# Kernel optimization log

Measured on AMD Instinct MI355X. Metric: run time of the kernel, lower is better.

## Reference

```python
import jax, jax.numpy as jnp
import numpy as np

N = 50000   # nodes
E = 1600000 # edges
G = 256     # graphs
EPS = 1e-5  # batchnorm eps (torch default)


def _bn(h, g, b):
    # training-mode BatchNorm1d: biased batch stats
    m = h.mean(0)
    v = h.var(0)
    return (h - m) * jax.lax.rsqrt(v + EPS) * g + b


def _mlp(h, W1, b1, g, be, W2, b2):
    # Lin -> BN -> ReLU -> Lin
    h = jax.nn.relu(_bn(h @ W1 + b1, g, be))
    return h @ W2 + b2


def _scatter_mean(v, idx, n):
    s = jax.ops.segment_sum(v, idx, num_segments=n)
    c = jax.ops.segment_sum(jnp.ones((v.shape[0], 1), v.dtype), idx, num_segments=n)
    return s / jnp.maximum(c, 1.0)


def setup_inputs() -> dict:
    key = jax.random.key(0)
    ks = iter(jax.random.split(key, 32))
    d = {}
    d["x"] = jax.random.normal(next(ks), (N, 48), dtype=jnp.float32)
    d["edge_index"] = jax.random.randint(next(ks), (2, E), 0, N, dtype=jnp.int64)
    d["batch"] = jnp.sort(jax.random.randint(next(ks), (N,), 0, G, dtype=jnp.int64))

    def lin(k, fin, fout):
        kw, kb = jax.random.split(k)
        s = 1.0 / np.sqrt(fin)
        return (jax.random.uniform(kw, (fin, fout), jnp.float32, -s, s),
                jax.random.uniform(kb, (fout,), jnp.float32, -s, s))

    # input BatchNorm1d(48)
    d["bn_g"] = jnp.ones((48,), jnp.float32)
    d["bn_b"] = jnp.zeros((48,), jnp.float32)

    def mlp_params(prefix, fin, fmid, fout):
        W1, b1 = lin(next(ks), fin, fmid)
        W2, b2 = lin(next(ks), fmid, fout)
        d[prefix + "_W1"], d[prefix + "_b1"] = W1, b1
        d[prefix + "_g"] = jnp.ones((fmid,), jnp.float32)
        d[prefix + "_be"] = jnp.zeros((fmid,), jnp.float32)
        d[prefix + "_W2"], d[prefix + "_b2"] = W2, b2

    mlp_params("e", 96, 128, 128)    # EdgeBlock
    mlp_params("n1", 176, 128, 128)  # NodeBlock mlp1
    mlp_params("n2", 176, 128, 128)  # NodeBlock mlp2
    mlp_params("gl", 128, 128, 2)    # GlobalBlock
    return d


def reference(x, edge_index, batch, bn_g, bn_b,
              e_W1, e_b1, e_g, e_be, e_W2, e_b2,
              n1_W1, n1_b1, n1_g, n1_be, n1_W2, n1_b2,
              n2_W1, n2_b1, n2_g, n2_be, n2_W2, n2_b2,
              gl_W1, gl_b1, gl_g, gl_be, gl_W2, gl_b2):
    x = _bn(x, bn_g, bn_b)
    row, col = edge_index[0], edge_index[1]
    # EdgeBlock: cat(src, dest) -> MLP
    edge_attr = _mlp(jnp.concatenate([x[row], x[col]], axis=1),
                     e_W1, e_b1, e_g, e_be, e_W2, e_b2)
    # NodeBlock: cat(x[row], edge_attr) -> mlp1 -> scatter_mean(col) -> cat(x,.) -> mlp2
    m = _mlp(jnp.concatenate([x[row], edge_attr], axis=1),
             n1_W1, n1_b1, n1_g, n1_be, n1_W2, n1_b2)
    agg = _scatter_mean(m, col, N)
    x2 = _mlp(jnp.concatenate([x, agg], axis=1),
              n2_W1, n2_b1, n2_g, n2_be, n2_W2, n2_b2)
    # GlobalBlock: scatter_mean over graphs -> MLP -> [G, 2]
    u = _scatter_mean(x2, batch, G)
    u = _mlp(u, gl_W1, gl_b1, gl_g, gl_be, gl_W2, gl_b2)
    return u
```

## Files before the change

### kernel.cpp

```cpp
#include <hip/hip_runtime.h>
#include <hip/hip_bf16.h>
#include <stdint.h>

#define DEV static __device__ __forceinline__

constexpr int N_ = 50000;
constexpr int E_ = 1600000;
constexpr int G_ = 256;

typedef __attribute__((ext_vector_type(8))) short short8;
typedef __attribute__((ext_vector_type(4))) float float4v;

DEV uint16_t f2bf(float f){
  uint32_t u = __float_as_uint(f);
  uint32_t r = (u + 0x7fffu + ((u >> 16) & 1u)) >> 16;
  return (uint16_t)r;
}
DEV float bf2f(uint16_t v){ return __uint_as_float((uint32_t)v << 16); }
DEV void unpack2(uint32_t p, float& a, float& b){
  a = __uint_as_float(p << 16);
  b = __uint_as_float(p & 0xffff0000u);
}
DEV uint32_t pack2(float a, float b){
  return (uint32_t)f2bf(a) | ((uint32_t)f2bf(b) << 16);
// ... 196 lines not shown
    float4v wv = *(const float4v*)&W[k][cg*4];
    #pragma unroll
    for (int i = 0; i < 4; i++)
      #pragma unroll
      for (int j = 0; j < 4; j++)
        acc[i][j] += xv[i]*wv[j];
  }
  #pragma unroll
  for (int i = 0; i < 4; i++){
    int n = n0 + ng*4 + i;
    if (n >= N_) continue;
    uint2 pv;
    pv.x = pack2(acc[i][0], acc[i][1]);
    pv.y = pack2(acc[i][2], acc[i][3]);
    *(uint2*)&Bn[(size_t)n*128 + cg*4] = pv;
  }
}

__global__ void k_bnfin(const float* __restrict__ statsR, int reps, const float* __restrict__ g,
                        const float* __restrict__ be, float* __restrict__ s_out, float* __restrict__ t_out,
                        float inv_n){
  int c = threadIdx.x;
  if (c >= 128) return;
  float sm = 0.f, sq = 0.f;
  for (int r = 0; r < reps; r++){ sm += statsR[r*256 + c]; sq += statsR[r*256 + 128 + c]; }
  float m = sm * inv_n;
  float v = sq * inv_n - m*m;
  float s = g[c] / sqrtf(v + 1e-5f);
  s_out[c] = s;
  t_out[c] = be[c] - m*s;
}


__global__ __launch_bounds__(512, 4) void k_estats2(
    const int2* __restrict__ rcs, const uint16_t* __restrict__ xn,
    const uint16_t* __restrict__ Bn, const uint16_t* __restrict__ W1t,
    float* __restrict__ estR){
  __shared__ __align__(16) uint16_t XNR[128*68];
  __shared__ __align__(16) uint16_t Hh[128*132];
  __shared__ __align__(16) uint16_t Wb[128*68];
  __shared__ __align__(16) uint16_t Bseg[32*128];
  __shared__ float lst[256];
  __shared__ int ssid[128], scol[128], scseg[32];
  __shared__ int sm_w0, snseg;
  const int t = threadIdx.x;
  const long i0 = (long)blockIdx.x * 128;
  const int lane = t & 63, w = t >> 6;
  const int m = lane & 15, quad = lane >> 4;
  uint32_t* XNRd = (uint32_t*)XNR;
  uint32_t* Wd = (uint32_t*)Wb;
  uint32_t* Hd = (uint32_t*)Hh;

  if (t < 256) lst[t] = 0.f;

  int sid_loc = 0; bool bnd = false; int myc = 0;
  if (t < 128){
    myc = rcs[i0 + t].y;
    int prevc = (t > 0) ? rcs[i0 + t - 1].y : myc;
    bnd = (t > 0) && (myc != prevc);
    unsigned long long mask = __ballot(bnd);
    sid_loc = __popcll(mask << (63 - lane));
    scol[t] = myc;
    if (t == 63) sm_w0 = sid_loc;
  }
  {
    int e = t >> 2, q = t & 3;
    int r = rcs[i0 + e].x;
    const uint2* src = (const uint2*)(xn + (size_t)r*48 + q*12);
    uint2 d0 = src[0], d1 = src[1], d2 = src[2];
    uint32_t* dst = XNRd + e*34 + q*6;
    *(uint2*)dst = d0; *(uint2*)(dst+2) = d1; *(uint2*)(dst+4) = d2;
  }
  for (int idx = t; idx < 1024; idx += 512){
    int rr = idx >> 3;
    XNRd[rr*34 + 24 + (idx & 7)] = 0;
  }
  {
    const uint32_t* src = (const uint32_t*)W1t;
    for (int idx = t; idx < 4096; idx += 512){
      int n = idx >> 5, d = idx & 31;
      Wd[n*34 + d] = src[n*32 + d];
    }
  }
  __syncthreads();
  if (t >= 64 && t < 128) sid_loc += sm_w0;
  if (t < 128){
    ssid[t] = sid_loc;
    if ((bnd || t == 0) && sid_loc < 32) scseg[sid_loc] = myc;
    if (t == 127) snseg = sid_loc + 1;
  }
  __syncthreads();
  {
    int ns = snseg; if (ns > 32) ns = 32;
    uint32_t* Bsegd = (uint32_t*)Bseg;
    const uint32_t* Bnd = (const uint32_t*)Bn;
    for (int idx = t; idx < ns*64; idx += 512){
      int s = idx >> 6, d = idx & 63;
      Bsegd[s*64 + d] = Bnd[(size_t)scseg[s]*64 + d];
    }
  }
  __syncthreads();

  float4v acc[8];
  #pragma unroll
  for (int nt = 0; nt < 8; nt++){ acc[nt][0]=0.f; acc[nt][1]=0.f; acc[nt][2]=0.f; acc[nt][3]=0.f; }
  {
    const uint16_t* aptr = XNR + (w*16 + m)*68 + quad*8;
    const uint16_t* bbase = Wb + m*68 + quad*8;
    #pragma unroll
    for (int ks = 0; ks < 2; ks++){
      short8 af = lds_load8(aptr + ks*32);
      #pragma unroll
      for (int nt = 0; nt < 8; nt++){
        short8 bf = lds_load8(bbase + nt*16*68 + ks*32);
        acc[nt] = __builtin_amdgcn_mfma_f32_16x16x32_bf16(af, bf, acc[nt], 0, 0, 0);
      }
    }
  }
  {
    int elb = w*16 + quad*4;
    int sids[4];
    #pragma unroll
    for (int reg = 0; reg < 4; reg++) sids[reg] = ssid[elb + reg];
    #pragma unroll
    for (int nt = 0; nt < 8; nt++){
      int col = nt*16 + m;
      #pragma unroll
      for (int reg = 0; reg < 4; reg++){
        float b = (sids[reg] < 32) ? bf2f(Bseg[sids[reg]*128 + col])
                                   : bf2f(Bn[(size_t)scol[elb+reg]*128 + col]);
        Hh[(elb+reg)*132 + col] = f2bf(acc[nt][reg] + b);
      }
    }
  }
  __syncthreads();
  {
    int cp = t & 63, eg = t >> 6;
    float ss0=0,qq0=0,ss1=0,qq1=0;
    #pragma unroll
    for (int it = 0; it < 16; it++){
      int e = it*8 + eg;
      uint32_t ph = Hd[e*66 + cp];
      float h0,h1; unpack2(ph,h0,h1);
      ss0 += h0; qq0 += h0*h0; ss1 += h1; qq1 += h1*h1;
    }
    atomicAdd(&lst[2*cp], ss0);
    atomicAdd(&lst[2*cp+1], ss1);
    atomicAdd(&lst[128+2*cp], qq0);
    atomicAdd(&lst[128+2*cp+1], qq1);
  }
  __syncthreads();
  if (t < 256) atomicAdd(&estR[(blockIdx.x & 63)*256 + t], lst[t]);
}

__global__ __launch_bounds__(512, 4) void k_epass0(
    const int2* __restrict__ rcs, const uint16_t* __restrict__ xn,
    const uint16_t* __restrict__ Bn, const uint16_t* __restrict__ W1t,
    const uint16_t* __restrict__ Mt, const uint16_t* __restrict__ N1t,
    const float* __restrict__ se, const float* __restrict__ te,
    float* __restrict__ n1R){
  __shared__ __align__(16) uint16_t XNR[128*68];
  __shared__ __align__(16) uint16_t Hh[128*132];
  __shared__ __align__(16) uint16_t Wb[128*68];
  __shared__ __align__(16) uint16_t Bseg[32*128];
  __shared__ float sete[256];
  __shared__ float lst[256];
  __shared__ int ssid[128], scol[128], scseg[32];
  __shared__ int sm_w0, snseg;
  const int t = threadIdx.x;
  const long i0 = (long)blockIdx.x * 128;
  const int lane = t & 63, w = t >> 6;
  const int m = lane & 15, quad = lane >> 4;
  uint32_t* XNRd = (uint32_t*)XNR;
  uint32_t* Wd = (uint32_t*)Wb;
  uint32_t* Hd = (uint32_t*)Hh;

  if (t < 256) lst[t] = 0.f;
  if (t < 128){ sete[t] = se[t]; sete[128 + t] = te[t]; }

  int sid_loc = 0; bool bnd = false; int myc = 0;
  if (t < 128){
    myc = rcs[i0 + t].y;
    int prevc = (t > 0) ? rcs[i0 + t - 1].y : myc;
    bnd = (t > 0) && (myc != prevc);
    unsigned long long mask = __ballot(bnd);
    sid_loc = __popcll(mask << (63 - lane));
    scol[t] = myc;
    if (t == 63) sm_w0 = sid_loc;
  }
  {
    int e = t >> 2, q = t & 3;
    int r = rcs[i0 + e].x;
    const uint2* src = (const uint2*)(xn + (size_t)r*48 + q*12);
    uint2 d0 = src[0], d1 = src[1], d2 = src[2];
    uint32_t* dst = XNRd + e*34 + q*6;
    *(uint2*)dst = d0; *(uint2*)(dst+2) = d1; *(uint2*)(dst+4) = d2;
  }
  for (int idx = t; idx < 1024; idx += 512){
    int rr = idx >> 3;
    XNRd[rr*34 + 24 + (idx & 7)] = 0;
  }
  {
    const uint32_t* src = (const uint32_t*)W1t;
    for (int idx = t; idx < 4096; idx += 512){
      int n = idx >> 5, d = idx & 31;
      Wd[n*34 + d] = src[n*32 + d];
    }
  }
  __syncthreads();
  if (t >= 64 && t < 128) sid_loc += sm_w0;
  if (t < 128){
    ssid[t] = sid_loc;
    if ((bnd || t == 0) && sid_loc < 32) scseg[sid_loc] = myc;
    if (t == 127) snseg = sid_loc + 1;
  }
  __syncthreads();
  {
    int ns = snseg; if (ns > 32) ns = 32;
    uint32_t* Bsegd = (uint32_t*)Bseg;
    const uint32_t* Bnd = (const uint32_t*)Bn;
    for (int idx = t; idx < ns*64; idx += 512){
      int s = idx >> 6, d = idx & 63;
      Bsegd[s*64 + d] = Bnd[(size_t)scseg[s]*64 + d];
    }
  }
  __syncthreads();

  float4v acc[8];
  #pragma unroll
  for (int nt = 0; nt < 8; nt++){ acc[nt][0]=0.f; acc[nt][1]=0.f; acc[nt][2]=0.f; acc[nt][3]=0.f; }
  {
    const uint16_t* aptr = XNR + (w*16 + m)*68 + quad*8;
    const uint16_t* bbase = Wb + m*68 + quad*8;
    #pragma unroll
    for (int ks = 0; ks < 2; ks++){
      short8 af = lds_load8(aptr + ks*32);
      #pragma unroll
      for (int nt = 0; nt < 8; nt++){
        short8 bf = lds_load8(bbase + nt*16*68 + ks*32);
        acc[nt] = __builtin_amdgcn_mfma_f32_16x16x32_bf16(af, bf, acc[nt], 0, 0, 0);
      }
    }
  }
  {
    int elb = w*16 + quad*4;
    int sids[4];
    #pragma unroll
    for (int reg = 0; reg < 4; reg++) sids[reg] = ssid[elb + reg];
    #pragma unroll
    for (int nt = 0; nt < 8; nt++){
      int col = nt*16 + m;
      float sc = sete[col], tc = sete[128 + col];
      #pragma unroll
      for (int reg = 0; reg < 4; reg++){
        float b = (sids[reg] < 32) ? bf2f(Bseg[sids[reg]*128 + col])
                                   : bf2f(Bn[(size_t)scol[elb+reg]*128 + col]);
        float v = fmaxf(0.f, (acc[nt][reg] + b)*sc + tc);
        Hh[(elb+reg)*132 + col] = f2bf(v);
      }
    }
  }

  float4v acc2[8];
  #pragma unroll
  for (int nt = 0; nt < 8; nt++){ acc2[nt][0]=0.f; acc2[nt][1]=0.f; acc2[nt][2]=0.f; acc2[nt][3]=0.f; }
  const uint32_t* Mtd = (const uint32_t*)Mt;
  const uint32_t* N1td = (const uint32_t*)N1t;
  for (int s = 0; s < 3; s++){
    __syncthreads();
    for (int idx = t; idx < 4096; idx += 512){
      int n = idx >> 5, d = idx & 31;
      Wd[n*34 + d] = (s < 2) ? Mtd[n*64 + s*32 + d] : N1td[n*32 + d];
    }
    __syncthreads();
    const uint16_t* a2 = (s == 2) ? (XNR + (w*16 + m)*68 + quad*8)
                                  : (Hh + (w*16 + m)*132 + s*64 + quad*8);
    const uint16_t* bbase = Wb + m*68 + quad*8;
    #pragma unroll
    for (int ks = 0; ks < 2; ks++){
      short8 af = lds_load8(a2 + ks*32);
      #pragma unroll
      for (int nt = 0; nt < 8; nt++){
        short8 bf = lds_load8(bbase + nt*16*68 + ks*32);
        acc2[nt] = __builtin_amdgcn_mfma_f32_16x16x32_bf16(af, bf, acc2[nt], 0, 0, 0);
      }
    }
  }
  __syncthreads();
  {
    int elb = w*16 + quad*4;
    #pragma unroll
    for (int nt = 0; nt < 8; nt++)
      #pragma unroll
      for (int reg = 0; reg < 4; reg++)
        Hh[(elb+reg)*132 + nt*16 + m] = f2bf(acc2[nt][reg]);
  }
  __syncthreads();
  {
    int cp = t & 63, eg = t >> 6;
    float ss0=0,qq0=0,ss1=0,qq1=0;
    #pragma unroll
    for (int it = 0; it < 16; it++){
      int e = it*8 + eg;
      uint32_t ph = Hd[e*66 + cp];
      float h0,h1; unpack2(ph,h0,h1);
      ss0 += h0; qq0 += h0*h0; ss1 += h1; qq1 += h1*h1;
    }
    atomicAdd(&lst[2*cp], ss0);
    atomicAdd(&lst[2*cp+1], ss1);
    atomicAdd(&lst[128+2*cp], qq0);
    atomicAdd(&lst[128+2*cp+1], qq1);
  }
  __syncthreads();
  if (t < 256) atomicAdd(&n1R[(blockIdx.x & 63)*256 + t], lst[t]);
}

__global__ __launch_bounds__(512, 4) void k_epass1(
    const int2* __restrict__ rcs, const uint16_t* __restrict__ xn,
    const uint16_t* __restrict__ Bn, const uint16_t* __restrict__ W1t,
    const uint16_t* __restrict__ Mt, const uint16_t* __restrict__ N1t,
    const float* __restrict__ se, const float* __restrict__ te,
    const float* __restrict__ sn1, const float* __restrict__ tn1,
    float* __restrict__ aggf){
  __shared__ __align__(16) uint16_t XNR[128*68];
  __shared__ __align__(16) uint16_t Hh[128*132];
  __shared__ __align__(16) uint16_t Wb[128*68];
  __shared__ __align__(16) uint16_t Bseg[32*128];
  __shared__ float sete[256];
  __shared__ int ssid[128], scol[128], scseg[32];
  __shared__ int sm_w0, snseg;
  const int t = threadIdx.x;
  const long i0 = (long)blockIdx.x * 128;
  const int lane = t & 63, w = t >> 6;
  const int m = lane & 15, quad = lane >> 4;
  uint32_t* XNRd = (uint32_t*)XNR;
  uint32_t* Wd = (uint32_t*)Wb;
  uint32_t* Hd = (uint32_t*)Hh;
  float* segacc = (float*)Wb;

  if (t < 128){ sete[t] = se[t]; sete[128 + t] = te[t]; }

  int sid_loc = 0; bool bnd = false; int myc = 0;
  if (t < 128){
    myc = rcs[i0 + t].y;
    int prevc = (t > 0) ? rcs[i0 + t - 1].y : myc;
    bnd = (t > 0) && (myc != prevc);
    unsigned long long mask = __ballot(bnd);
    sid_loc = __popcll(mask << (63 - lane));
    scol[t] = myc;
    if (t == 63) sm_w0 = sid_loc;
  }
  {
    int e = t >> 2, q = t & 3;
    int r = rcs[i0 + e].x;
    const uint2* src = (const uint2*)(xn + (size_t)r*48 + q*12);
    uint2 d0 = src[0], d1 = src[1], d2 = src[2];
    uint32_t* dst = XNRd + e*34 + q*6;
    *(uint2*)dst = d0; *(uint2*)(dst+2) = d1; *(uint2*)(dst+4) = d2;
  }
  for (int idx = t; idx < 1024; idx += 512){
    int rr = idx >> 3;
    XNRd[rr*34 + 24 + (idx & 7)] = 0;
  }
  {
    const uint32_t* src = (const uint32_t*)W1t;
    for (int idx = t; idx < 4096; idx += 512){
      int n = idx >> 5, d = idx & 31;
      Wd[n*34 + d] = src[n*32 + d];
    }
  }
  __syncthreads();
  if (t >= 64 && t < 128) sid_loc += sm_w0;
  if (t < 128){
    ssid[t] = sid_loc;
    if ((bnd || t == 0) && sid_loc < 32) scseg[sid_loc] = myc;
    if (t == 127) snseg = sid_loc + 1;
  }
  __syncthreads();
  {
    int ns = snseg; if (ns > 32) ns = 32;
    uint32_t* Bsegd = (uint32_t*)Bseg;
    const uint32_t* Bnd = (const uint32_t*)Bn;
    for (int idx = t; idx < ns*64; idx += 512){
      int s = idx >> 6, d = idx & 63;
      Bsegd[s*64 + d] = Bnd[(size_t)scseg[s]*64 + d];
    }
  }
  __syncthreads();

  float4v acc[8];
  #pragma unroll
  for (int nt = 0; nt < 8; nt++){ acc[nt][0]=0.f; acc[nt][1]=0.f; acc[nt][2]=0.f; acc[nt][3]=0.f; }
  {
    const uint16_t* aptr = XNR + (w*16 + m)*68 + quad*8;
    const uint16_t* bbase = Wb + m*68 + quad*8;
    #pragma unroll
    for (int ks = 0; ks < 2; ks++){
      short8 af = lds_load8(aptr + ks*32);
      #pragma unroll
      for (int nt = 0; nt < 8; nt++){
        short8 bf = lds_load8(bbase + nt*16*68 + ks*32);
        acc[nt] = __builtin_amdgcn_mfma_f32_16x16x32_bf16(af, bf, acc[nt], 0, 0, 0);
      }
    }
  }
  {
    int elb = w*16 + quad*4;
    int sids[4];
    #pragma unroll
    for (int reg = 0; reg < 4; reg++) sids[reg] = ssid[elb + reg];
    #pragma unroll
    for (int nt = 0; nt < 8; nt++){
      int col = nt*16 + m;
      float sc = sete[col], tc = sete[128 + col];
      #pragma unroll
      for (int reg = 0; reg < 4; reg++){
        float b = (sids[reg] < 32) ? bf2f(Bseg[sids[reg]*128 + col])
                                   : bf2f(Bn[(size_t)scol[elb+reg]*128 + col]);
        float v = fmaxf(0.f, (acc[nt][reg] + b)*sc + tc);
        Hh[(elb+reg)*132 + col] = f2bf(v);
      }
    }
  }

  float4v acc2[8];
  #pragma unroll
  for (int nt = 0; nt < 8; nt++){ acc2[nt][0]=0.f; acc2[nt][1]=0.f; acc2[nt][2]=0.f; acc2[nt][3]=0.f; }
  const uint32_t* Mtd = (const uint32_t*)Mt;
  const uint32_t* N1td = (const uint32_t*)N1t;
  for (int s = 0; s < 3; s++){
    __syncthreads();
    for (int idx = t; idx < 4096; idx += 512){
      int n = idx >> 5, d = idx & 31;
      Wd[n*34 + d] = (s < 2) ? Mtd[n*64 + s*32 + d] : N1td[n*32 + d];
    }
    __syncthreads();
    const uint16_t* a2 = (s == 2) ? (XNR + (w*16 + m)*68 + quad*8)
                                  : (Hh + (w*16 + m)*132 + s*64 + quad*8);
    const uint16_t* bbase = Wb + m*68 + quad*8;
    #pragma unroll
    for (int ks = 0; ks < 2; ks++){
      short8 af = lds_load8(a2 + ks*32);
      #pragma unroll
      for (int nt = 0; nt < 8; nt++){
        short8 bf = lds_load8(bbase + nt*16*68 + ks*32);
        acc2[nt] = __builtin_amdgcn_mfma_f32_16x16x32_bf16(af, bf, acc2[nt], 0, 0, 0);
      }
    }
  }
  __syncthreads();
  {
    int elb = w*16 + quad*4;
    #pragma unroll
    for (int nt = 0; nt < 8; nt++)
      #pragma unroll
      for (int reg = 0; reg < 4; reg++)
        Hh[(elb+reg)*132 + nt*16 + m] = f2bf(acc2[nt][reg]);
  }
  if (t < 128){ sete[t] = sn1[t]; sete[128 + t] = tn1[t]; }
  for (int idx = t; idx < 32*128; idx += 512) segacc[idx] = 0.f;
  __syncthreads();

  {
    int cp = t & 63, eg = t >> 6;
    float s0 = sete[2*cp], s1 = sete[2*cp+1];
    float b0 = sete[128+2*cp], b1 = sete[128+2*cp+1];
    int nseg = snseg;
    bool lp = (nseg <= 32);
    int cursid = ssid[eg*16];
    int curcol = scol[eg*16];
    float r0 = 0.f, r1 = 0.f;
    for (int it = 0; it < 16; it++){
      int e = eg*16 + it;
      uint32_t ph = Hd[e*66 + cp];
      float h0,h1; unpack2(ph,h0,h1);
      float v0 = fmaxf(0.f, h0*s0 + b0);
      float v1 = fmaxf(0.f, h1*s1 + b1);
      int sid = ssid[e];
      if (sid != cursid){
        if (lp){ atomicAdd(&segacc[cursid*128 + 2*cp], r0); atomicAdd(&segacc[cursid*128 + 2*cp+1], r1); }
        else { atomicAdd(&aggf[(size_t)curcol*128 + 2*cp], r0); atomicAdd(&aggf[(size_t)curcol*128 + 2*cp+1], r1); }
        cursid = sid; curcol = scol[e]; r0 = 0.f; r1 = 0.f;
      }
      r0 += v0; r1 += v1;
    }
    if (lp){ atomicAdd(&segacc[cursid*128 + 2*cp], r0); atomicAdd(&segacc[cursid*128 + 2*cp+1], r1); }
    else { atomicAdd(&aggf[(size_t)curcol*128 + 2*cp], r0); atomicAdd(&aggf[(size_t)curcol*128 + 2*cp+1], r1); }
    __syncthreads();
    if (lp){
      for (int idx = t; idx < nseg*64; idx += 512){
        int s = idx >> 6, cpp = idx & 63;
        float v0 = segacc[s*128 + 2*cpp], v1 = segacc[s*128 + 2*cpp+1];
        int c = scseg[s];
        float* dst = &aggf[(size_t)c*128 + 2*cpp];
        if (s == 0 || s == nseg - 1){ atomicAdd(dst, v0); atomicAdd(dst+1, v1); }
        else { dst[0] = v0; dst[1] = v1; }
      }
    }
  }
}

__global__ __launch_bounds__(256) void k_n2(const float* __restrict__ x,
    const float* __restrict__ sx, const float* __restrict__ tx,
    const float* __restrict__ aggf, const float* __restrict__ invc,
    const float* __restrict__ Wc, const float* __restrict__ c1, const int* __restrict__ counts,
    float* __restrict__ hn2, float* __restrict__ n2R){
  __shared__ float xT[44][36];
  __shared__ float wT[44][128];
  __shared__ float lst[256];
  int t = threadIdx.x;
  int n0 = blockIdx.x * 32;
  int cg = t & 31, ng = t >> 5;
  lst[t] = 0.f;
  float acc[4][4] = {{0.f}};
  for (int kc = 0; kc < 176; kc += 44){
    __syncthreads();
    for (int idx = t; idx < 32*44; idx += 256){
      int r = idx / 44, k = idx % 44;
      int n = n0 + r, kk = kc + k;
      float v = 0.f;
      if (n < N_){
        if (kk < 48) v = x[(size_t)n*48 + kk] * sx[kk] + tx[kk];
        else         v = aggf[(size_t)n*128 + (kk - 48)] * invc[n];
      }
      xT[k][r] = v;
    }
    for (int idx = t; idx < 44*128; idx += 256){
      int k = idx >> 7, c = idx & 127;
      wT[k][c] = Wc[(kc + k)*128 + c];
    }
    __syncthreads();
// ... 132 lines not shown
  int* offs = (int*)take((N_+1)*4);
  int* cur  = (int*)take(N_*4);
  int* goff = (int*)take(257*4);
  int* bsum = (int*)take(64*4);
  int* boff = (int*)take(64*4);
  uint16_t* Mt  = (uint16_t*)take(128*128*2);
  uint16_t* W1t = (uint16_t*)take(128*64*2);
  uint16_t* N1t = (uint16_t*)take(128*64*2);
  uint16_t* xn  = (uint16_t*)take((size_t)N_*48*2);
  uint16_t* Bn  = (uint16_t*)take((size_t)N_*128*2);
  float* aggf  = (float*)take((size_t)N_*128*4);
  float* hn2   = (float*)take((size_t)N_*128*4);
  int2* rcs = (int2*)take((size_t)E_*8);

  if (off > ws_size) return;

  hipMemsetAsync(zone, 0, ZONE_WORDS*4, stream);
  hipMemsetAsync(aggf, 0, (size_t)N_*128*4, stream);

  const int NB = (N_ + 1023) / 1024;
  hipLaunchKernelGGL(k_xstats, dim3(252), dim3(256), 0, stream, x, xstats);
  hipLaunchKernelGGL(k_hist, dim3((E_+255)/256), dim3(256), 0, stream, ei, counts);
  hipLaunchKernelGGL(k_xfin, dim3(1), dim3(64), 0, stream, xstats, bn_g, bn_b, sx, tx);
  hipLaunchKernelGGL(k_scanA, dim3(NB), dim3(256), 0, stream, counts, bsum);
  hipLaunchKernelGGL(k_scanB, dim3(1), dim3(64), 0, stream, bsum, boff, offs, NB);
  hipLaunchKernelGGL(k_scanC, dim3(NB), dim3(256), 0, stream, counts, boff, offs, cur);
  hipLaunchKernelGGL(k_place, dim3((E_+255)/256), dim3(256), 0, stream, ei, cur, rcs);
  hipLaunchKernelGGL(k_invc, dim3((N_+255)/256), dim3(256), 0, stream, counts, invc);
  hipLaunchKernelGGL(k_wprep, dim3(281), dim3(256), 0, stream,
                     eW1, eW2, n1W1, n1W2, n2W1, n2W2, glW1, n1b2, n2b2,
                     Mt, Wcomb, M3, c1, c3, W1t, N1t);
  hipLaunchKernelGGL(k_nodegemm, dim3((N_+31)/32), dim3(256), 0, stream,
                     x, sx, tx, eW1, Bn, xn);
  hipLaunchKernelGGL(k_estats2, dim3(E_/128), dim3(512), 0, stream,
                     rcs, xn, Bn, W1t, estR);
  hipLaunchKernelGGL(k_bnfin, dim3(1), dim3(128), 0, stream, estR, 64, e_g, e_be, se, te, 1.f/(float)E_);
  hipLaunchKernelGGL(k_epass0, dim3(E_/128), dim3(512), 0, stream,
                     rcs, xn, Bn, W1t, Mt, N1t, se, te, n1R);
  hipLaunchKernelGGL(k_bnfin, dim3(1), dim3(128), 0, stream, n1R, 64, n1_g, n1_be, sn1, tn1, 1.f/(float)E_);
  hipLaunchKernelGGL(k_epass1, dim3(E_/128), dim3(512), 0, stream,
                     rcs, xn, Bn, W1t, Mt, N1t, se, te, sn1, tn1, aggf);
  hipLaunchKernelGGL(k_n2, dim3((N_+31)/32), dim3(256), 0, stream,
                     x, sx, tx, aggf, invc, Wcomb, c1, counts, hn2, n2R);
  hipLaunchKernelGGL(k_bnfin, dim3(1), dim3(128), 0, stream, n2R, 64, n2_g, n2_be, sn2, tn2, 1.f/(float)N_);
  hipLaunchKernelGGL(k_goff, dim3(1), dim3(256), 0, stream, batch, goff);
  hipLaunchKernelGGL(k_gmean, dim3(256), dim3(128), 0, stream, hn2, goff, sn2, tn2, gmean);
  hipLaunchKernelGGL(k_hg, dim3(128), dim3(256), 0, stream, gmean, M3, c3, goff, hg, gls);
  hipLaunchKernelGGL(k_bnfin, dim3(1), dim3(128), 0, stream, gls, 1, gl_g, gl_be, sgl, tgl, 1.f/(float)G_);
  hipLaunchKernelGGL(k_out, dim3(2), dim3(256), 0, stream, hg, sgl, tgl, glW2, glb2, out);
}
```

Before: 1.656 ms.

## Shrink edge-kernel tiles to 64 edges and fuse xn/N1 GEMM into first stage

The three edge-pass kernels now process 64 edges per 256-thread block instead of 128 per 512. This cuts shared memory per block, removes several block-wide barriers and lets each wave own its 16 rows through the stats and scatter phases. In epass0/epass1 the N1 projection of x[row] is computed together with the W1 GEMM from a combined weight buffer, and the M weights are loaded once as a full K=128 panel rather than in three staged chunks. Epass1 drops the shared-memory segment accumulator and atomically adds per-wave segment partials straight to global memory. That may raise global atomic traffic, and weight staging is now repeated across twice as many blocks.

```diff
diff --git a/kernel.cpp b/kernel.cpp
--- a/kernel.cpp
+++ b/kernel.cpp
@@ -252,71 +252,56 @@
 }
 
 
-__global__ __launch_bounds__(512, 4) void k_estats2(
+__global__ __launch_bounds__(256, 4) void k_estats2(
     const int2* __restrict__ rcs, const uint16_t* __restrict__ xn,
     const uint16_t* __restrict__ Bn, const uint16_t* __restrict__ W1t,
     float* __restrict__ estR){
-  __shared__ __align__(16) uint16_t XNR[128*68];
-  __shared__ __align__(16) uint16_t Hh[128*132];
-  __shared__ __align__(16) uint16_t Wb[128*68];
-  __shared__ __align__(16) uint16_t Bseg[32*128];
+  __shared__ __align__(16) uint16_t bufA[64*132];
+  __shared__ __align__(16) uint16_t bufW[128*68];
+  __shared__ __align__(16) uint16_t Bseg[8*128];
   __shared__ float lst[256];
-  __shared__ int ssid[128], scol[128], scseg[32];
-  __shared__ int sm_w0, snseg;
-  const int t = threadIdx.x;
-  const long i0 = (long)blockIdx.x * 128;
-  const int lane = t & 63, w = t >> 6;
+  __shared__ int ssid[64], scol[64], scseg[8];
+  const int t = threadIdx.x, lane = t & 63, w = t >> 6;
   const int m = lane & 15, quad = lane >> 4;
-  uint32_t* XNRd = (uint32_t*)XNR;
-  uint32_t* Wd = (uint32_t*)Wb;
-  uint32_t* Hd = (uint32_t*)Hh;
-
-  if (t < 256) lst[t] = 0.f;
-
-  int sid_loc = 0; bool bnd = false; int myc = 0;
-  if (t < 128){
-    myc = rcs[i0 + t].y;
-    int prevc = (t > 0) ? rcs[i0 + t - 1].y : myc;
-    bnd = (t > 0) && (myc != prevc);
+  const int e = t >> 2, q = t & 3;
+  const long i0 = (long)blockIdx.x * 64;
+  uint32_t* bufAd = (uint32_t*)bufA;
+
+  int r = rcs[i0 + e].x;
+  uint2 g0, g1, g2, g3;
+  if (q < 3){
+    const uint2* src = (const uint2*)(xn + (size_t)r*48 + q*16);
+    g0 = src[0]; g1 = src[1]; g2 = src[2]; g3 = src[3];
+  }
+  lst[t] = 0.f;
+  {
+    uint32_t* dst = bufAd + e*66 + q*8;
+    if (q < 3){ *(uint2*)dst = g0; *(uint2*)(dst+2) = g1; *(uint2*)(dst+4) = g2; *(uint2*)(dst+6) = g3; }
+    else { uint2 z = make_uint2(0,0); *(uint2*)dst = z; *(uint2*)(dst+2) = z; *(uint2*)(dst+4) = z; *(uint2*)(dst+6) = z; }
+  }
+  if (t < 64){
+    int myc = rcs[i0 + t].y;
+    int prevc = __shfl_up(myc, 1);
+    bool bnd = (lane > 0) && (myc != prevc);
     unsigned long long mask = __ballot(bnd);
-    sid_loc = __popcll(mask << (63 - lane));
-    scol[t] = myc;
-    if (t == 63) sm_w0 = sid_loc;
-  }
-  {
-    int e = t >> 2, q = t & 3;
-    int r = rcs[i0 + e].x;
-    const uint2* src = (const uint2*)(xn + (size_t)r*48 + q*12);
-    uint2 d0 = src[0], d1 = src[1], d2 = src[2];
-    uint32_t* dst = XNRd + e*34 + q*6;
-    *(uint2*)dst = d0; *(uint2*)(dst+2) = d1; *(uint2*)(dst+4) = d2;
-  }
-  for (int idx = t; idx < 1024; idx += 512){
-    int rr = idx >> 3;
-    XNRd[rr*34 + 24 + (idx & 7)] = 0;
-  }
-  {
-    const uint32_t* src = (const uint32_t*)W1t;
-    for (int idx = t; idx < 4096; idx += 512){
-      int n = idx >> 5, d = idx & 31;
-      Wd[n*34 + d] = src[n*32 + d];
-    }
-  }
-  __syncthreads();
-  if (t >= 64 && t < 128) sid_loc += sm_w0;
-  if (t < 128){
-    ssid[t] = sid_loc;
-    if ((bnd || t == 0) && sid_loc < 32) scseg[sid_loc] = myc;
-    if (t == 127) snseg = sid_loc + 1;
-  }
-  __syncthreads();
-  {
-    int ns = snseg; if (ns > 32) ns = 32;
+    int sid = __popcll(mask << (63 - lane));
+    int ns = __popcll(mask) + 1;
+    ssid[t] = sid; scol[t] = myc;
+    if ((bnd || lane == 0) && sid < 8) scseg[sid] = myc;
+    int nsc = (ns < 8) ? ns : 8;
+    const uint32_t* Bnd = (const uint32_t*)Bn;
     uint32_t* Bsegd = (uint32_t*)Bseg;
-    const uint32_t* Bnd = (const uint32_t*)Bn;
-    for (int idx = t; idx < ns*64; idx += 512){
+    for (int idx = lane; idx < nsc*64; idx += 64){
       int s = idx >> 6, d = idx & 63;
       Bsegd[s*64 + d] = Bnd[(size_t)scseg[s]*64 + d];
+    }
+  }
+  {
+    const uint32_t* W1d = (const uint32_t*)W1t;
+    uint32_t* Wd = (uint32_t*)bufW;
+    for (int idx = t; idx < 4096; idx += 256){
+      int n = idx >> 5, d = idx & 31;
+      Wd[n*34 + d] = W1d[n*32 + d];
     }
   }
   __syncthreads();
@@ -325,43 +310,41 @@
   #pragma unroll
   for (int nt = 0; nt < 8; nt++){ acc[nt][0]=0.f; acc[nt][1]=0.f; acc[nt][2]=0.f; acc[nt][3]=0.f; }
   {
-    const uint16_t* aptr = XNR + (w*16 + m)*68 + quad*8;
-    const uint16_t* bbase = Wb + m*68 + quad*8;
+    const uint16_t* aX = bufA + (w*16 + m)*132 + quad*8;
+    const uint16_t* bb = bufW + m*68 + quad*8;
     #pragma unroll
     for (int ks = 0; ks < 2; ks++){
-      short8 af = lds_load8(aptr + ks*32);
+      short8 af = lds_load8(aX + ks*32);
       #pragma unroll
       for (int nt = 0; nt < 8; nt++){
-        short8 bf = lds_load8(bbase + nt*16*68 + ks*32);
+        short8 bf = lds_load8(bb + nt*16*68 + ks*32);
         acc[nt] = __builtin_amdgcn_mfma_f32_16x16x32_bf16(af, bf, acc[nt], 0, 0, 0);
       }
     }
   }
   {
-    int elb = w*16 + quad*4;
-    int sids[4];
-    #pragma unroll
-    for (int reg = 0; reg < 4; reg++) sids[reg] = ssid[elb + reg];
+    const int elb = w*16 + quad*4;
+    int sid_r[4], col_r[4];
+    #pragma unroll
+    for (int reg = 0; reg < 4; reg++){ sid_r[reg] = ssid[elb + reg]; col_r[reg] = scol[elb + reg]; }
     #pragma unroll
     for (int nt = 0; nt < 8; nt++){
       int col = nt*16 + m;
       #pragma unroll
       for (int reg = 0; reg < 4; reg++){
-        float b = (sids[reg] < 32) ? bf2f(Bseg[sids[reg]*128 + col])
-                                   : bf2f(Bn[(size_t)scol[elb+reg]*128 + col]);
-        Hh[(elb+reg)*132 + col] = f2bf(acc[nt][reg] + b);
-      }
-    }
-  }
-  __syncthreads();
-  {
-    int cp = t & 63, eg = t >> 6;
+        float b = (sid_r[reg] < 8) ? bf2f(Bseg[sid_r[reg]*128 + col])
+                                   : bf2f(Bn[(size_t)col_r[reg]*128 + col]);
+        bufA[(elb + reg)*132 + col] = f2bf(acc[nt][reg] + b);
+      }
+    }
+  }
+  {
+    int cp = lane;
     float ss0=0,qq0=0,ss1=0,qq1=0;
     #pragma unroll
     for (int it = 0; it < 16; it++){
-      int e = it*8 + eg;
-      uint32_t ph = Hd[e*66 + cp];
-      float h0,h1; unpack2(ph,h0,h1);
+      uint32_t ph = bufAd[(w*16 + it)*66 + cp];
+      float h0, h1; unpack2(ph, h0, h1);
       ss0 += h0; qq0 += h0*h0; ss1 += h1; qq1 += h1*h1;
     }
     atomicAdd(&lst[2*cp], ss0);
@@ -370,160 +353,150 @@
     atomicAdd(&lst[128+2*cp+1], qq1);
   }
   __syncthreads();
-  if (t < 256) atomicAdd(&estR[(blockIdx.x & 63)*256 + t], lst[t]);
-}
-
-__global__ __launch_bounds__(512, 4) void k_epass0(
+  atomicAdd(&estR[(blockIdx.x & 63)*256 + t], lst[t]);
+}
+
+__global__ __launch_bounds__(256, 3) void k_epass0(
     const int2* __restrict__ rcs, const uint16_t* __restrict__ xn,
     const uint16_t* __restrict__ Bn, const uint16_t* __restrict__ W1t,
-    const uint16_t* __restrict__ Mt, const uint16_t* __restrict__ N1t,
+    const uint16_t* __restrict__ N1t, const uint16_t* __restrict__ Mt,
     const float* __restrict__ se, const float* __restrict__ te,
     float* __restrict__ n1R){
-  __shared__ __align__(16) uint16_t XNR[128*68];
-  __shared__ __align__(16) uint16_t Hh[128*132];
-  __shared__ __align__(16) uint16_t Wb[128*68];
-  __shared__ __align__(16) uint16_t Bseg[32*128];
-  __shared__ float sete[256];
-  __shared__ float lst[256];
-  __shared__ int ssid[128], scol[128], scseg[32];
-  __shared__ int sm_w0, snseg;
-  const int t = threadIdx.x;
-  const long i0 = (long)blockIdx.x * 128;
-  const int lane = t & 63, w = t >> 6;
+  __shared__ __align__(16) uint16_t bufA[64*132];
+  __shared__ __align__(16) uint16_t bufB[128*132];
+  __shared__ __align__(16) uint16_t Bseg[8*128];
+  __shared__ int ssid[64], scol[64], scseg[8];
+  const int t = threadIdx.x, lane = t & 63, w = t >> 6;
   const int m = lane & 15, quad = lane >> 4;
-  uint32_t* XNRd = (uint32_t*)XNR;
-  uint32_t* Wd = (uint32_t*)Wb;
-  uint32_t* Hd = (uint32_t*)Hh;
-
-  if (t < 256) lst[t] = 0.f;
-  if (t < 128){ sete[t] = se[t]; sete[128 + t] = te[t]; }
-
-  int sid_loc = 0; bool bnd = false; int myc = 0;
-  if (t < 128){
-    myc = rcs[i0 + t].y;
-    int prevc = (t > 0) ? rcs[i0 + t - 1].y : myc;
-    bnd = (t > 0) && (myc != prevc);
+  const int e = t >> 2, q = t & 3;
+  const long i0 = (long)blockIdx.x * 64;
+  uint32_t* bufAd = (uint32_t*)bufA;
+  uint32_t* bufBd = (uint32_t*)bufB;
+  float* lst = (float*)Bseg;
+
+  float se_v[8], te_v[8];
+  #pragma unroll
+  for (int nt = 0; nt < 8; nt++){ se_v[nt] = se[nt*16 + m]; te_v[nt] = te[nt*16 + m]; }
+
+  int r = rcs[i0 + e].x;
+  uint2 g0, g1, g2, g3;
+  if (q < 3){
+    const uint2* src = (const uint2*)(xn + (size_t)r*48 + q*16);
+    g0 = src[0]; g1 = src[1]; g2 = src[2]; g3 = src[3];
+  }
+  {
+    uint32_t* dst = bufAd + e*66 + q*8;
+    if (q < 3){ *(uint2*)dst = g0; *(uint2*)(dst+2) = g1; *(uint2*)(dst+4) = g2; *(uint2*)(dst+6) = g3; }
+    else { uint2 z = make_uint2(0,0); *(uint2*)dst = z; *(uint2*)(dst+2) = z; *(uint2*)(dst+4) = z; *(uint2*)(dst+6) = z; }
+  }
+  if (t < 64){
+    int myc = rcs[i0 + t].y;
+    int prevc = __shfl_up(myc, 1);
+    bool bnd = (lane > 0) && (myc != prevc);
     unsigned long long mask = __ballot(bnd);
-    sid_loc = __popcll(mask << (63 - lane));
-    scol[t] = myc;
-    if (t == 63) sm_w0 = sid_loc;
-  }
-  {
-    int e = t >> 2, q = t & 3;
-    int r = rcs[i0 + e].x;
-    const uint2* src = (const uint2*)(xn + (size_t)r*48 + q*12);
-    uint2 d0 = src[0], d1 = src[1], d2 = src[2];
-    uint32_t* dst = XNRd + e*34 + q*6;
-    *(uint2*)dst = d0; *(uint2*)(dst+2) = d1; *(uint2*)(dst+4) = d2;
-  }
-  for (int idx = t; idx < 1024; idx += 512){
-    int rr = idx >> 3;
-    XNRd[rr*34 + 24 + (idx & 7)] = 0;
-  }
-  {
-    const uint32_t* src = (const uint32_t*)W1t;
-    for (int idx = t; idx < 4096; idx += 512){
-      int n = idx >> 5, d = idx & 31;
-      Wd[n*34 + d] = src[n*32 + d];
-    }
-  }
-  __syncthreads();
-  if (t >= 64 && t < 128) sid_loc += sm_w0;
-  if (t < 128){
-    ssid[t] = sid_loc;
-    if ((bnd || t == 0) && sid_loc < 32) scseg[sid_loc] = myc;
-    if (t == 127) snseg = sid_loc + 1;
-  }
-  __syncthreads();
-  {
-    int ns = snseg; if (ns > 32) ns = 32;
+    int sid = __popcll(mask << (63 - lane));
+    int ns = __popcll(mask) + 1;
+    ssid[t] = sid; scol[t] = myc;
+    if ((bnd || lane == 0) && sid < 8) scseg[sid] = myc;
+    int nsc = (ns < 8) ? ns : 8;
+    const uint32_t* Bnd = (const uint32_t*)Bn;
     uint32_t* Bsegd = (uint32_t*)Bseg;
-    const uint32_t* Bnd = (const uint32_t*)Bn;
-    for (int idx = t; idx < ns*64; idx += 512){
+    for (int idx = lane; idx < nsc*64; idx += 64){
       int s = idx >> 6, d = idx & 63;
       Bsegd[s*64 + d] = Bnd[(size_t)scseg[s]*64 + d];
     }
   }
-  __syncthreads();
-
-  float4v acc[8];
+  {
+    const uint32_t* W1d = (const uint32_t*)W1t;
+    const uint32_t* N1d = (const uint32_t*)N1t;
+    for (int idx = t; idx < 8192; idx += 256){
+      int n = idx >> 6, d = idx & 63;
+      bufBd[n*66 + d] = (d < 32) ? W1d[n*32 + d] : N1d[n*32 + (d - 32)];
+    }
+  }
+  __syncthreads();
+
+  float4v acc1[8], acc2[8];
   #pragma unroll
-  for (int nt = 0; nt < 8; nt++){ acc[nt][0]=0.f; acc[nt][1]=0.f; acc[nt][2]=0.f; acc[nt][3]=0.f; }
-  {
-    const uint16_t* aptr = XNR + (w*16 + m)*68 + quad*8;
-    const uint16_t* bbase = Wb + m*68 + quad*8;
+  for (int nt = 0; nt < 8; nt++){
+    acc1[nt][0]=0.f; acc1[nt][1]=0.f; acc1[nt][2]=0.f; acc1[nt][3]=0.f;
+    acc2[nt][0]=0.f; acc2[nt][1]=0.f; acc2[nt][2]=0.f; acc2[nt][3]=0.f;
+  }
+  {
+    const uint16_t* aX = bufA + (w*16 + m)*132 + quad*8;
+    const uint16_t* b1 = bufB + m*132 + quad*8;
+    const uint16_t* b2 = bufB + m*132 + 64 + quad*8;
     #pragma unroll
     for (int ks = 0; ks < 2; ks++){
-      short8 af = lds_load8(aptr + ks*32);
+      short8 af = lds_load8(aX + ks*32);
       #pragma unroll
       for (int nt = 0; nt < 8; nt++){
-        short8 bf = lds_load8(bbase + nt*16*68 + ks*32);
-        acc[nt] = __builtin_amdgcn_mfma_f32_16x16x32_bf16(af, bf, acc[nt], 0, 0, 0);
-      }
-    }
-  }
-  {
-    int elb = w*16 + quad*4;
-    int sids[4];
-    #pragma unroll
-    for (int reg = 0; reg < 4; reg++) sids[reg] = ssid[elb + reg];
+        short8 bf = lds_load8(b1 + nt*16*132 + ks*32);
+        acc1[nt] = __builtin_amdgcn_mfma_f32_16x16x32_bf16(af, bf, acc1[nt], 0, 0, 0);
+      }
+      #pragma unroll
+      for (int nt = 0; nt < 8; nt++){
+        short8 bf = lds_load8(b2 + nt*16*132 + ks*32);
+        acc2[nt] = __builtin_amdgcn_mfma_f32_16x16x32_bf16(af, bf, acc2[nt], 0, 0, 0);
+      }
+    }
+  }
+  {
+    const int elb = w*16 + quad*4;
+    int sid_r[4], col_r[4];
+    #pragma unroll
+    for (int reg = 0; reg < 4; reg++){ sid_r[reg] = ssid[elb + reg]; col_r[reg] = scol[elb + reg]; }
     #pragma unroll
     for (int nt = 0; nt < 8; nt++){
       int col = nt*16 + m;
-      float sc = sete[col], tc = sete[128 + col];
       #pragma unroll
       for (int reg = 0; reg < 4; reg++){
-        float b = (sids[reg] < 32) ? bf2f(Bseg[sids[reg]*128 + col])
-                                   : bf2f(Bn[(size_t)scol[elb+reg]*128 + col]);
-        float v = fmaxf(0.f, (acc[nt][reg] + b)*sc + tc);
-        Hh[(elb+reg)*132 + col] = f2bf(v);
-      }
-    }
-  }
-
-  float4v acc2[8];
-  #pragma unroll
-  for (int nt = 0; nt < 8; nt++){ acc2[nt][0]=0.f; acc2[nt][1]=0.f; acc2[nt][2]=0.f; acc2[nt][3]=0.f; }
-  const uint32_t* Mtd = (const uint32_t*)Mt;
-  const uint32_t* N1td = (const uint32_t*)N1t;
-  for (int s = 0; s < 3; s++){
-    __syncthreads();
-    for (int idx = t; idx < 4096; idx += 512){
-      int n = idx >> 5, d = idx & 31;
-      Wd[n*34 + d] = (s < 2) ? Mtd[n*64 + s*32 + d] : N1td[n*32 + d];
-    }
-    __syncthreads();
-    const uint16_t* a2 = (s == 2) ? (XNR + (w*16 + m)*68 + quad*8)
-                                  : (Hh + (w*16 + m)*132 + s*64 + quad*8);
-    const uint16_t* bbase = Wb + m*68 + quad*8;
-    #pragma unroll
-    for (int ks = 0; ks < 2; ks++){
-      short8 af = lds_load8(a2 + ks*32);
+        float b = (sid_r[reg] < 8) ? bf2f(Bseg[sid_r[reg]*128 + col])
+                                   : bf2f(Bn[(size_t)col_r[reg]*128 + col]);
+        float v = fmaxf(0.f, (acc1[nt][reg] + b)*se_v[nt] + te_v[nt]);
+        bufA[(elb + reg)*132 + col] = f2bf(v);
+      }
+    }
+  }
+  __syncthreads();
+  {
+    const uint32_t* Mtd = (const uint32_t*)Mt;
+    for (int idx = t; idx < 8192; idx += 256){
+      int n = idx >> 6, d = idx & 63;
+      bufBd[n*66 + d] = Mtd[n*64 + d];
+    }
+  }
+  lst[t] = 0.f;
+  __syncthreads();
+
+  {
+    const uint16_t* aH = bufA + (w*16 + m)*132 + quad*8;
+    const uint16_t* bb = bufB + m*132 + quad*8;
+    #pragma unroll
+    for (int ks = 0; ks < 4; ks++){
+      short8 af = lds_load8(aH + ks*32);
       #pragma unroll
       for (int nt = 0; nt < 8; nt++){
-        short8 bf = lds_load8(bbase + nt*16*68 + ks*32);
+        short8 bf = lds_load8(bb + nt*16*132 + ks*32);
         acc2[nt] = __builtin_amdgcn_mfma_f32_16x16x32_bf16(af, bf, acc2[nt], 0, 0, 0);
       }
     }
   }
-  __syncthreads();
-  {
-    int elb = w*16 + quad*4;
+  {
+    const int elb = w*16 + quad*4;
     #pragma unroll
     for (int nt = 0; nt < 8; nt++)
       #pragma unroll
       for (int reg = 0; reg < 4; reg++)
-        Hh[(elb+reg)*132 + nt*16 + m] = f2bf(acc2[nt][reg]);
-  }
-  __syncthreads();
-  {
-    int cp = t & 63, eg = t >> 6;
+        bufA[(elb + reg)*132 + nt*16 + m] = f2bf(acc2[nt][reg]);
+  }
+  {
+    int cp = lane;
     float ss0=0,qq0=0,ss1=0,qq1=0;
     #pragma unroll
     for (int it = 0; it < 16; it++){
-      int e = it*8 + eg;
-      uint32_t ph = Hd[e*66 + cp];
-      float h0,h1; unpack2(ph,h0,h1);
+      uint32_t ph = bufAd[(w*16 + it)*66 + cp];
+      float h0, h1; unpack2(ph, h0, h1);
       ss0 += h0; qq0 += h0*h0; ss1 += h1; qq1 += h1*h1;
     }
     atomicAdd(&lst[2*cp], ss0);
@@ -532,191 +505,168 @@
     atomicAdd(&lst[128+2*cp+1], qq1);
   }
   __syncthreads();
-  if (t < 256) atomicAdd(&n1R[(blockIdx.x & 63)*256 + t], lst[t]);
-}
-
-__global__ __launch_bounds__(512, 4) void k_epass1(
+  atomicAdd(&n1R[(blockIdx.x & 63)*256 + t], lst[t]);
+}
+
+__global__ __launch_bounds__(256, 3) void k_epass1(
     const int2* __restrict__ rcs, const uint16_t* __restrict__ xn,
     const uint16_t* __restrict__ Bn, const uint16_t* __restrict__ W1t,
-    const uint16_t* __restrict__ Mt, const uint16_t* __restrict__ N1t,
+    const uint16_t* __restrict__ N1t, const uint16_t* __restrict__ Mt,
     const float* __restrict__ se, const float* __restrict__ te,
     const float* __restrict__ sn1, const float* __restrict__ tn1,
     float* __restrict__ aggf){
-  __shared__ __align__(16) uint16_t XNR[128*68];
-  __shared__ __align__(16) uint16_t Hh[128*132];
-  __shared__ __align__(16) uint16_t Wb[128*68];
-  __shared__ __align__(16) uint16_t Bseg[32*128];
-  __shared__ float sete[256];
-  __shared__ int ssid[128], scol[128], scseg[32];
-  __shared__ int sm_w0, snseg;
-  const int t = threadIdx.x;
-  const long i0 = (long)blockIdx.x * 128;
-  const int lane = t & 63, w = t >> 6;
+  __shared__ __align__(16) uint16_t bufA[64*132];
+  __shared__ __align__(16) uint16_t bufB[128*132];
+  __shared__ __align__(16) uint16_t Bseg[8*128];
+  __shared__ int ssid[64], scol[64], scseg[8];
+  const int t = threadIdx.x, lane = t & 63, w = t >> 6;
   const int m = lane & 15, quad = lane >> 4;
-  uint32_t* XNRd = (uint32_t*)XNR;
-  uint32_t* Wd = (uint32_t*)Wb;
-  uint32_t* Hd = (uint32_t*)Hh;
-  float* segacc = (float*)Wb;
-
-  if (t < 128){ sete[t] = se[t]; sete[128 + t] = te[t]; }
-
-  int sid_loc = 0; bool bnd = false; int myc = 0;
-  if (t < 128){
-    myc = rcs[i0 + t].y;
-    int prevc = (t > 0) ? rcs[i0 + t - 1].y : myc;
-    bnd = (t > 0) && (myc != prevc);
+  const int e = t >> 2, q = t & 3;
+  const long i0 = (long)blockIdx.x * 64;
+  uint32_t* bufAd = (uint32_t*)bufA;
+  uint32_t* bufBd = (uint32_t*)bufB;
+
+  float se_v[8], te_v[8], sn_v[8], tn_v[8];
+  #pragma unroll
+  for (int nt = 0; nt < 8; nt++){
+    se_v[nt] = se[nt*16 + m]; te_v[nt] = te[nt*16 + m];
+    sn_v[nt] = sn1[nt*16 + m]; tn_v[nt] = tn1[nt*16 + m];
+  }
+
+  int r = rcs[i0 + e].x;
+  uint2 g0, g1, g2, g3;
+  if (q < 3){
+    const uint2* src = (const uint2*)(xn + (size_t)r*48 + q*16);
+    g0 = src[0]; g1 = src[1]; g2 = src[2]; g3 = src[3];
+  }
+  {
+    uint32_t* dst = bufAd + e*66 + q*8;
+    if (q < 3){ *(uint2*)dst = g0; *(uint2*)(dst+2) = g1; *(uint2*)(dst+4) = g2; *(uint2*)(dst+6) = g3; }
+    else { uint2 z = make_uint2(0,0); *(uint2*)dst = z; *(uint2*)(dst+2) = z; *(uint2*)(dst+4) = z; *(uint2*)(dst+6) = z; }
+  }
+  if (t < 64){
+    int myc = rcs[i0 + t].y;
+    int prevc = __shfl_up(myc, 1);
+    bool bnd = (lane > 0) && (myc != prevc);
     unsigned long long mask = __ballot(bnd);
-    sid_loc = __popcll(mask << (63 - lane));
-    scol[t] = myc;
-    if (t == 63) sm_w0 = sid_loc;
-  }
-  {
-    int e = t >> 2, q = t & 3;
-    int r = rcs[i0 + e].x;
-    const uint2* src = (const uint2*)(xn + (size_t)r*48 + q*12);
-    uint2 d0 = src[0], d1 = src[1], d2 = src[2];
-    uint32_t* dst = XNRd + e*34 + q*6;
-    *(uint2*)dst = d0; *(uint2*)(dst+2) = d1; *(uint2*)(dst+4) = d2;
-  }
-  for (int idx = t; idx < 1024; idx += 512){
-    int rr = idx >> 3;
-    XNRd[rr*34 + 24 + (idx & 7)] = 0;
-  }
-  {
-    const uint32_t* src = (const uint32_t*)W1t;
-    for (int idx = t; idx < 4096; idx += 512){
-      int n = idx >> 5, d = idx & 31;
-      Wd[n*34 + d] = src[n*32 + d];
-    }
-  }
-  __syncthreads();
-  if (t >= 64 && t < 128) sid_loc += sm_w0;
-  if (t < 128){
-    ssid[t] = sid_loc;
-    if ((bnd || t == 0) && sid_loc < 32) scseg[sid_loc] = myc;
-    if (t == 127) snseg = sid_loc + 1;
-  }
-  __syncthreads();
-  {
-    int ns = snseg; if (ns > 32) ns = 32;
+    int sid = __popcll(mask << (63 - lane));
+    int ns = __popcll(mask) + 1;
+    ssid[t] = sid; scol[t] = myc;
+    if ((bnd || lane == 0) && sid < 8) scseg[sid] = myc;
+    int nsc = (ns < 8) ? ns : 8;
+    const uint32_t* Bnd = (const uint32_t*)Bn;
     uint32_t* Bsegd = (uint32_t*)Bseg;
-    const uint32_t* Bnd = (const uint32_t*)Bn;
-    for (int idx = t; idx < ns*64; idx += 512){
+    for (int idx = lane; idx < nsc*64; idx += 64){
       int s = idx >> 6, d = idx & 63;
       Bsegd[s*64 + d] = Bnd[(size_t)scseg[s]*64 + d];
     }
   }
-  __syncthreads();
-
-  float4v acc[8];
+  {
+    const uint32_t* W1d = (const uint32_t*)W1t;
+    const uint32_t* N1d = (const uint32_t*)N1t;
+    for (int idx = t; idx < 8192; idx += 256){
+      int n = idx >> 6, d = idx & 63;
+      bufBd[n*66 + d] = (d < 32) ? W1d[n*32 + d] : N1d[n*32 + (d - 32)];
+    }
+  }
+  __syncthreads();
+
+  float4v acc1[8], acc2[8];
   #pragma unroll
-  for (int nt = 0; nt < 8; nt++){ acc[nt][0]=0.f; acc[nt][1]=0.f; acc[nt][2]=0.f; acc[nt][3]=0.f; }
-  {
-    const uint16_t* aptr = XNR + (w*16 + m)*68 + quad*8;
-    const uint16_t* bbase = Wb + m*68 + quad*8;
+  for (int nt = 0; nt < 8; nt++){
+    acc1[nt][0]=0.f; acc1[nt][1]=0.f; acc1[nt][2]=0.f; acc1[nt][3]=0.f;
+    acc2[nt][0]=0.f; acc2[nt][1]=0.f; acc2[nt][2]=0.f; acc2[nt][3]=0.f;
+  }
+  {
+    const uint16_t* aX = bufA + (w*16 + m)*132 + quad*8;
+    const uint16_t* b1 = bufB + m*132 + quad*8;
+    const uint16_t* b2 = bufB + m*132 + 64 + quad*8;
     #pragma unroll
     for (int ks = 0; ks < 2; ks++){
-      short8 af = lds_load8(aptr + ks*32);
+      short8 af = lds_load8(aX + ks*32);
       #pragma unroll
       for (int nt = 0; nt < 8; nt++){
-        short8 bf = lds_load8(bbase + nt*16*68 + ks*32);
-        acc[nt] = __builtin_amdgcn_mfma_f32_16x16x32_bf16(af, bf, acc[nt], 0, 0, 0);
-      }
-    }
-  }
-  {
-    int elb = w*16 + quad*4;
-    int sids[4];
-    #pragma unroll
-    for (int reg = 0; reg < 4; reg++) sids[reg] = ssid[elb + reg];
+        short8 bf = lds_load8(b1 + nt*16*132 + ks*32);
+        acc1[nt] = __builtin_amdgcn_mfma_f32_16x16x32_bf16(af, bf, acc1[nt], 0, 0, 0);
+      }
+      #pragma unroll
+      for (int nt = 0; nt < 8; nt++){
+        short8 bf = lds_load8(b2 + nt*16*132 + ks*32);
+        acc2[nt] = __builtin_amdgcn_mfma_f32_16x16x32_bf16(af, bf, acc2[nt], 0, 0, 0);
+      }
+    }
+  }
+  {
+    const int elb = w*16 + quad*4;
+    int sid_r[4], col_r[4];
+    #pragma unroll
+    for (int reg = 0; reg < 4; reg++){ sid_r[reg] = ssid[elb + reg]; col_r[reg] = scol[elb + reg]; }
     #pragma unroll
     for (int nt = 0; nt < 8; nt++){
       int col = nt*16 + m;
-      float sc = sete[col], tc = sete[128 + col];
       #pragma unroll
       for (int reg = 0; reg < 4; reg++){
-        float b = (sids[reg] < 32) ? bf2f(Bseg[sids[reg]*128 + col])
-                                   : bf2f(Bn[(size_t)scol[elb+reg]*128 + col]);
-        float v = fmaxf(0.f, (acc[nt][reg] + b)*sc + tc);
-        Hh[(elb+reg)*132 + col] = f2bf(v);
-      }
-    }
-  }
-
-  float4v acc2[8];
-  #pragma unroll
-  for (int nt = 0; nt < 8; nt++){ acc2[nt][0]=0.f; acc2[nt][1]=0.f; acc2[nt][2]=0.f; acc2[nt][3]=0.f; }
-  const uint32_t* Mtd = (const uint32_t*)Mt;
-  const uint32_t* N1td = (const uint32_t*)N1t;
-  for (int s = 0; s < 3; s++){
-    __syncthreads();
-    for (int idx = t; idx < 4096; idx += 512){
-      int n = idx >> 5, d = idx & 31;
-      Wd[n*34 + d] = (s < 2) ? Mtd[n*64 + s*32 + d] : N1td[n*32 + d];
-    }
-    __syncthreads();
-    const uint16_t* a2 = (s == 2) ? (XNR + (w*16 + m)*68 + quad*8)
-                                  : (Hh + (w*16 + m)*132 + s*64 + quad*8);
-    const uint16_t* bbase = Wb + m*68 + quad*8;
-    #pragma unroll
-    for (int ks = 0; ks < 2; ks++){
-      short8 af = lds_load8(a2 + ks*32);
+        float b = (sid_r[reg] < 8) ? bf2f(Bseg[sid_r[reg]*128 + col])
+                                   : bf2f(Bn[(size_t)col_r[reg]*128 + col]);
+        float v = fmaxf(0.f, (acc1[nt][reg] + b)*se_v[nt] + te_v[nt]);
+        bufA[(elb + reg)*132 + col] = f2bf(v);
+      }
+    }
+  }
+  __syncthreads();
+  {
+    const uint32_t* Mtd = (const uint32_t*)Mt;
+    for (int idx = t; idx < 8192; idx += 256){
+      int n = idx >> 6, d = idx & 63;
+      bufBd[n*66 + d] = Mtd[n*64 + d];
+    }
+  }
+  __syncthreads();
+
+  {
+    const uint16_t* aH = bufA + (w*16 + m)*132 + quad*8;
+    const uint16_t* bb = bufB + m*132 + quad*8;
+    #pragma unroll
+    for (int ks = 0; ks < 4; ks++){
+      short8 af = lds_load8(aH + ks*32);
       #pragma unroll
       for (int nt = 0; nt < 8; nt++){
-        short8 bf = lds_load8(bbase + nt*16*68 + ks*32);
+        short8 bf = lds_load8(bb + nt*16*132 + ks*32);
         acc2[nt] = __builtin_amdgcn_mfma_f32_16x16x32_bf16(af, bf, acc2[nt], 0, 0, 0);
       }
     }
   }
-  __syncthreads();
-  {
-    int elb = w*16 + quad*4;
-    #pragma unroll
-    for (int nt = 0; nt < 8; nt++)
-      #pragma unroll
-      for (int reg = 0; reg < 4; reg++)
-        Hh[(elb+reg)*132 + nt*16 + m] = f2bf(acc2[nt][reg]);
-  }
-  if (t < 128){ sete[t] = sn1[t]; sete[128 + t] = tn1[t]; }
-  for (int idx = t; idx < 32*128; idx += 512) segacc[idx] = 0.f;
-  __syncthreads();
-
-  {
-    int cp = t & 63, eg = t >> 6;
-    float s0 = sete[2*cp], s1 = sete[2*cp+1];
-    float b0 = sete[128+2*cp], b1 = sete[128+2*cp+1];
-    int nseg = snseg;
-    bool lp = (nseg <= 32);
-    int cursid = ssid[eg*16];
-    int curcol = scol[eg*16];
+  {
+    const int elb = w*16 + quad*4;
+    #pragma unroll
+    for (int nt = 0; nt < 8; nt++){
+      #pragma unroll
+      for (int reg = 0; reg < 4; reg++){
+        float v = fmaxf(0.f, acc2[nt][reg]*sn_v[nt] + tn_v[nt]);
+        bufA[(elb + reg)*132 + nt*16 + m] = f2bf(v);
+      }
+    }
+  }
+  {
+    int cp = lane;
+    int e0g = w*16;
+    int cursid = ssid[e0g];
+    int curcol = scol[e0g];
     float r0 = 0.f, r1 = 0.f;
     for (int it = 0; it < 16; it++){
-      int e = eg*16 + it;
-      uint32_t ph = Hd[e*66 + cp];
-      float h0,h1; unpack2(ph,h0,h1);
-      float v0 = fmaxf(0.f, h0*s0 + b0);
-      float v1 = fmaxf(0.f, h1*s1 + b1);
-      int sid = ssid[e];
+      int ee = e0g + it;
+      uint32_t ph = bufAd[ee*66 + cp];
+      float v0, v1; unpack2(ph, v0, v1);
+      int sid = ssid[ee];
       if (sid != cursid){
-        if (lp){ atomicAdd(&segacc[cursid*128 + 2*cp], r0); atomicAdd(&segacc[cursid*128 + 2*cp+1], r1); }
-        else { atomicAdd(&aggf[(size_t)curcol*128 + 2*cp], r0); atomicAdd(&aggf[(size_t)curcol*128 + 2*cp+1], r1); }
-        cursid = sid; curcol = scol[e]; r0 = 0.f; r1 = 0.f;
+        atomicAdd(&aggf[(size_t)curcol*128 + 2*cp], r0);
+        atomicAdd(&aggf[(size_t)curcol*128 + 2*cp + 1], r1);
+        cursid = sid; curcol = scol[ee]; r0 = 0.f; r1 = 0.f;
       }
       r0 += v0; r1 += v1;
     }
-    if (lp){ atomicAdd(&segacc[cursid*128 + 2*cp], r0); atomicAdd(&segacc[cursid*128 + 2*cp+1], r1); }
-    else { atomicAdd(&aggf[(size_t)curcol*128 + 2*cp], r0); atomicAdd(&aggf[(size_t)curcol*128 + 2*cp+1], r1); }
-    __syncthreads();
-    if (lp){
-      for (int idx = t; idx < nseg*64; idx += 512){
-        int s = idx >> 6, cpp = idx & 63;
-        float v0 = segacc[s*128 + 2*cpp], v1 = segacc[s*128 + 2*cpp+1];
-        int c = scseg[s];
-        float* dst = &aggf[(size_t)c*128 + 2*cpp];
-        if (s == 0 || s == nseg - 1){ atomicAdd(dst, v0); atomicAdd(dst+1, v1); }
-        else { dst[0] = v0; dst[1] = v1; }
-      }
-    }
+    atomicAdd(&aggf[(size_t)curcol*128 + 2*cp], r0);
+    atomicAdd(&aggf[(size_t)curcol*128 + 2*cp + 1], r1);
   }
 }
 
@@ -915,14 +865,14 @@
                      Mt, Wcomb, M3, c1, c3, W1t, N1t);
   hipLaunchKernelGGL(k_nodegemm, dim3((N_+31)/32), dim3(256), 0, stream,
                      x, sx, tx, eW1, Bn, xn);
-  hipLaunchKernelGGL(k_estats2, dim3(E_/128), dim3(512), 0, stream,
+  hipLaunchKernelGGL(k_estats2, dim3(E_/64), dim3(256), 0, stream,
                      rcs, xn, Bn, W1t, estR);
   hipLaunchKernelGGL(k_bnfin, dim3(1), dim3(128), 0, stream, estR, 64, e_g, e_be, se, te, 1.f/(float)E_);
-  hipLaunchKernelGGL(k_epass0, dim3(E_/128), dim3(512), 0, stream,
-                     rcs, xn, Bn, W1t, Mt, N1t, se, te, n1R);
+  hipLaunchKernelGGL(k_epass0, dim3(E_/64), dim3(256), 0, stream,
+                     rcs, xn, Bn, W1t, N1t, Mt, se, te, n1R);
   hipLaunchKernelGGL(k_bnfin, dim3(1), dim3(128), 0, stream, n1R, 64, n1_g, n1_be, sn1, tn1, 1.f/(float)E_);
-  hipLaunchKernelGGL(k_epass1, dim3(E_/128), dim3(512), 0, stream,
-                     rcs, xn, Bn, W1t, Mt, N1t, se, te, sn1, tn1, aggf);
+  hipLaunchKernelGGL(k_epass1, dim3(E_/64), dim3(256), 0, stream,
+                     rcs, xn, Bn, W1t, N1t, Mt, se, te, sn1, tn1, aggf);
   hipLaunchKernelGGL(k_n2, dim3((N_+31)/32), dim3(256), 0, stream,
                      x, sx, tx, aggf, invc, Wcomb, c1, counts, hn2, n2R);
   hipLaunchKernelGGL(k_bnfin, dim3(1), dim3(128), 0, stream, n2R, 64, n2_g, n2_be, sn2, tn2, 1.f/(float)N_);
```

After: 1.664 ms. About the same (+0.5%).
